# Kernel tuning notes

Measured on AMD Instinct MI355X. Metric: run time of the kernel, lower is better.

## Reference

```python
import jax, jax.numpy as jnp
import numpy as np

NUM_GENES = 8192
NUM_SETS = 256
BATCH = 32
ALPHA = 0.25


def setup_inputs() -> dict:
    key = jax.random.key(0)
    k1, k2, k3 = jax.random.split(key, 3)
    R = jax.random.uniform(k1, (BATCH, NUM_GENES), dtype=jnp.float32)
    # S is a per-sample permutation of gene indices (sort order)
    S = jnp.argsort(jax.random.uniform(k2, (BATCH, NUM_GENES)), axis=1).astype(jnp.int32)
    W = jax.random.normal(k3, (NUM_SETS, NUM_GENES), dtype=jnp.float32)  # set_membership
    return {"R": R, "S": S, "W": W}


def _set_indicators(W):
    ind = jax.nn.sigmoid(W)  # (M, G)
    avg = ind.mean(axis=1, keepdims=True)
    return jnp.where(ind < avg * 0.3, ind * 0.01, ind)


def reference(R, S, W):
    batch, num_genes = R.shape
    ind = _set_indicators(W)                                   # (M, G)
    # gather indicators per sample's sort order: (B, M, G)
    sorted_ind = jnp.transpose(ind[:, S], (1, 0, 2))
    R_sorted = jnp.take_along_axis(R, S, axis=1)               # (B, G)
    clamped = jnp.clip(R_sorted[:, None, :] * sorted_ind, 1e-8, 1e4)
    wpos = clamped ** ALPHA                                    # (B, M, G)
    sum_pos = jnp.sum(wpos, axis=2, keepdims=True)
    cdf_pos = jnp.where(sum_pos > 1e-8,
                        jnp.cumsum(wpos, axis=2) / (sum_pos + 1e-10),
                        jnp.zeros_like(wpos))
    neg = (sorted_ind < 0.1).astype(R.dtype)                   # (B, M, G)
    sum_neg = jnp.sum(neg, axis=2, keepdims=True)
    cdf_neg = jnp.where(sum_neg > 1e-8,
                        jnp.cumsum(neg, axis=2) / (sum_neg + 1e-10),
                        jnp.zeros_like(neg))
    diff = (cdf_pos - cdf_neg) / num_genes
    return jnp.sum(diff, axis=2)                               # (B, M)
```

## Files before the change

### kernel.cpp

```cpp
#include <hip/hip_runtime.h>
#include <math.h>

constexpr int NG  = 8192;
constexpr int NM  = 256;
constexpr int NB  = 32;
constexpr int KR  = 128;
constexpr int NKB = NG / KR;


using bf16x8 = __attribute__((ext_vector_type(8))) short;
using f32x4  = __attribute__((ext_vector_type(4))) float;

__device__ __forceinline__ float sigmoidf(float x) {
  return __builtin_amdgcn_rcpf(1.0f + __builtin_amdgcn_exp2f(x * -1.442695041f));
}
__device__ __forceinline__ float qrtf(float x) {
  return __builtin_amdgcn_sqrtf(__builtin_amdgcn_sqrtf(x));
}
__device__ __forceinline__ short bfr(float f) {
  unsigned x = __float_as_uint(f);
  return (short)((x + 0x7fffu + ((x >> 16) & 1u)) >> 16);
}

__global__ __launch_bounds__(256) void k_prep(const int* __restrict__ S,
                                              const float* __restrict__ W,
                                              float* __restrict__ cf,
                                              float* __restrict__ thr,
                                              float* __restrict__ sumN) {
  const int tid = threadIdx.x;

  if (blockIdx.x < NM) {
    __shared__ float red[4];
    const int m = blockIdx.x;
    const float4* w4 = reinterpret_cast<const float4*>(W + (size_t)m * NG);
    float4 sg[8];
    float s = 0.f;
    #pragma unroll
    for (int q = 0; q < 8; ++q) {
      float4 v = w4[q * 256 + tid];
      sg[q] = make_float4(sigmoidf(v.x), sigmoidf(v.y), sigmoidf(v.z), sigmoidf(v.w));
      s += sg[q].x + sg[q].y + sg[q].z + sg[q].w;
    }
    #pragma unroll
    for (int off = 32; off > 0; off >>= 1) s += __shfl_xor(s, off, 64);
    if ((tid & 63) == 0) red[tid >> 6] = s;
    __syncthreads();
    const float tm = (red[0] + red[1] + red[2] + red[3]) * (0.3f / (float)NG);
    __syncthreads();
    float sn = 0.f;
    #pragma unroll
    for (int q = 0; q < 8; ++q) {
      float vv[4] = {sg[q].x, sg[q].y, sg[q].z, sg[q].w};
      #pragma unroll
      for (int j = 0; j < 4; ++j) {
        float v = vv[j];
        v = (v < tm) ? v * 0.01f : v;
        sn += (v < 0.1f) ? 1.f : 0.f;
      }
    }
    #pragma unroll
    for (int off = 32; off > 0; off >>= 1) sn += __shfl_xor(sn, off, 64);
    if ((tid & 63) == 0) red[tid >> 6] = sn;
    __syncthreads();
    if (tid == 0) { thr[m] = tm; sumN[m] = red[0] + red[1] + red[2] + red[3]; }
  } else {
    __shared__ float row[NG];
    const int b = blockIdx.x - NM;
    const int4* s4 = reinterpret_cast<const int4*>(S + (size_t)b * NG);
    #pragma unroll
    for (int q = 0; q < 8; ++q) {
      const int i = q * 256 + tid;
      const int4 g4 = s4[i];
      const int k = i * 4;
      row[g4.x] = (float)(NG - k);
      row[g4.y] = (float)(NG - (k + 1));
      row[g4.z] = (float)(NG - (k + 2));
      row[g4.w] = (float)(NG - (k + 3));
    }
    __syncthreads();
    float4* dst = reinterpret_cast<float4*>(cf + (size_t)b * NG);
    const float4* src = reinterpret_cast<const float4*>(row);
    #pragma unroll
    for (int q = 0; q < 8; ++q)
      dst[q * 256 + tid] = src[q * 256 + tid];
  }
}

__global__ __launch_bounds__(256) void k_mm(const float* __restrict__ W,
                                            const float* __restrict__ thr,
                                            const float* __restrict__ R,
                                            const float* __restrict__ cf,
                                            float* __restrict__ part) {
  const int tid  = threadIdx.x;
  const int kb   = blockIdx.x;
  const int mt   = blockIdx.y;
  const int wv   = tid >> 6;
  const int mw   = wv >> 1, bw = wv & 1;
  const int lane = tid & 63;
  const int lr   = lane & 15, lk = lane >> 4;

  const int m = mt * 32 + mw * 16 + lr;
  const int b = bw * 16 + lr;
  const float tm = thr[m];

  f32x4 accA = {0.f, 0.f, 0.f, 0.f};
  f32x4 accB = {0.f, 0.f, 0.f, 0.f};
  f32x4 accC = {0.f, 0.f, 0.f, 0.f};

  #pragma unroll
  for (int c = 0; c < KR / 32; ++c) {
    const int g = kb * KR + c * 32 + lk * 8;

    const float4 w0 = *reinterpret_cast<const float4*>(W + (size_t)m * NG + g);
    const float4 w1 = *reinterpret_cast<const float4*>(W + (size_t)m * NG + g + 4);
    const float wa[8] = {w0.x, w0.y, w0.z, w0.w, w1.x, w1.y, w1.z, w1.w};
    bf16x8 fia, fnf;
    #pragma unroll
    for (int e = 0; e < 8; ++e) {
      float v = sigmoidf(wa[e]);
      v = (v < tm) ? v * 0.01f : v;
      fia[e] = bfr(qrtf(v));
      fnf[e] = (v < 0.1f) ? (short)0x3F80 : (short)0;
    }

    const float4 r0 = *reinterpret_cast<const float4*>(R  + (size_t)b * NG + g);
    const float4 r1 = *reinterpret_cast<const float4*>(R  + (size_t)b * NG + g + 4);
    const float4 c0 = *reinterpret_cast<const float4*>(cf + (size_t)b * NG + g);
    const float4 c1 = *reinterpret_cast<const float4*>(cf + (size_t)b * NG + g + 4);
    const float rr[8] = {r0.x, r0.y, r0.z, r0.w, r1.x, r1.y, r1.z, r1.w};
    const float cc[8] = {c0.x, c0.y, c0.z, c0.w, c1.x, c1.y, c1.z, c1.w};
    bf16x8 fra, frc, fcf;
    #pragma unroll
    for (int e = 0; e < 8; ++e) {
      const float ra = qrtf(rr[e]);
      fra[e] = bfr(ra);
      frc[e] = bfr(ra * cc[e]);
      fcf[e] = bfr(cc[e]);
    }

    accA = __builtin_amdgcn_mfma_f32_16x16x32_bf16(fia, fra, accA, 0, 0, 0);
    accB = __builtin_amdgcn_mfma_f32_16x16x32_bf16(fia, frc, accB, 0, 0, 0);
    accC = __builtin_amdgcn_mfma_f32_16x16x32_bf16(fnf, fcf, accC, 0, 0, 0);
  }

  const int md = mt * 32 + mw * 16 + 4 * lk;
  const int bd = bw * 16 + lr;
  #pragma unroll
  for (int i = 0; i < 4; ++i) {
    part[((size_t)(kb * 3 + 0) * NM + md + i) * NB + bd] = accA[i];
    part[((size_t)(kb * 3 + 1) * NM + md + i) * NB + bd] = accB[i];
    part[((size_t)(kb * 3 + 2) * NM + md + i) * NB + bd] = accC[i];
  }
}

__global__ __launch_bounds__(256) void k_final(const float* __restrict__ part,
                                               const float* __restrict__ sumN,
                                               float* __restrict__ out) {
  __shared__ float rA[256], rB[256], rC[256];
  const int tid = threadIdx.x;
  const int m   = blockIdx.x;
  const int b   = tid & 31;
  const int kg  = tid >> 5;

  float sA = 0.f, sB = 0.f, sC = 0.f;
  #pragma unroll
  for (int t = 0; t < NKB / 8; ++t) {
    const int kb = kg * (NKB / 8) + t;
    const float* p = part + ((size_t)(kb * 3) * NM + m) * NB + b;
    sA += p[0];
    sB += p[(size_t)NM * NB];
    sC += p[2 * (size_t)NM * NB];
  }
  rA[tid] = sA; rB[tid] = sB; rC[tid] = sC;
  __syncthreads();
  if (tid < 128) { rA[tid] += rA[tid + 128]; rB[tid] += rB[tid + 128]; rC[tid] += rC[tid + 128]; }
  __syncthreads();
  if (tid < 64)  { rA[tid] += rA[tid + 64];  rB[tid] += rB[tid + 64];  rC[tid] += rC[tid + 64]; }
  __syncthreads();
  if (tid < 32) {
    const float a  = rA[tid] + rA[tid + 32];
    const float bb = rB[tid] + rB[tid + 32];
    const float c  = rC[tid] + rC[tid + 32];
    const float sN = sumN[m];
    out[(size_t)tid * NM + m] = (bb / (a + 1e-10f) - c / (sN + 1e-10f)) * (1.0f / (float)NG);
  }
}

extern "C" void kernel_launch(void* const* d_in, const int* in_sizes, int n_in,
                              void* d_out, int out_size, void* d_ws, size_t ws_size,
                              hipStream_t stream) {
  const float* R = (const float*)d_in[0];
  const int*   S = (const int*)d_in[1];
  const float* W = (const float*)d_in[2];
  float* out = (float*)d_out;

  char* ws = (char*)d_ws;
  float* cf   = (float*)ws;
  float* part = cf + (size_t)NB * NG;
  float* thr  = part + (size_t)NKB * 3 * NM * NB;
  float* sumN = thr + NM;

  k_prep <<<dim3(NM + NB), dim3(256), 0, stream>>>(S, W, cf, thr, sumN);
  k_mm   <<<dim3(NKB, NM / 32), dim3(256), 0, stream>>>(W, thr, R, cf, part);
  k_final<<<dim3(NM), dim3(256), 0, stream>>>(part, sumN, out);
}
```

Measured before the change: 22.36 us.

## Precompute packed bf16 operands in prep kernel and double K-chunk size

The prep kernel now computes the transformed set indicators (fourth root in bf16, negative flag packed into the sign bit) and the per-sample bf16 operands (rank fourth root, its product with the rank-based CDF weight, the rank itself). It writes them to workspace, so the matmul kernel only loads bf16 vectors and does bit masking before the MFMAs. This removes the sigmoid, threshold and fourth-root work that k_mm repeated for every m-tile and batch half, and halves the bytes it reads. K-block size goes from 128 to 256, halving the partial-sum traffic but also the number of k_mm blocks. The cost is extra global writes and reads of the packed buffers.

```diff
diff --git a/kernel.cpp b/kernel.cpp
--- a/kernel.cpp
+++ b/kernel.cpp
@@ -4,11 +4,12 @@
 constexpr int NG  = 8192;
 constexpr int NM  = 256;
 constexpr int NB  = 32;
-constexpr int KR  = 128;
+constexpr int KR  = 256;
 constexpr int NKB = NG / KR;
 
 
 using bf16x8 = __attribute__((ext_vector_type(8))) short;
+using s16x4  = __attribute__((ext_vector_type(4))) short;
 using f32x4  = __attribute__((ext_vector_type(4))) float;
 
 __device__ __forceinline__ float sigmoidf(float x) {
@@ -24,8 +25,9 @@
 
 __global__ __launch_bounds__(256) void k_prep(const int* __restrict__ S,
                                               const float* __restrict__ W,
-                                              float* __restrict__ cf,
-                                              float* __restrict__ thr,
+                                              const float* __restrict__ R,
+                                              unsigned short* __restrict__ pA,
+                                              unsigned short* __restrict__ pB,
                                               float* __restrict__ sumN) {
   const int tid = threadIdx.x;
 
@@ -46,23 +48,27 @@
     if ((tid & 63) == 0) red[tid >> 6] = s;
     __syncthreads();
     const float tm = (red[0] + red[1] + red[2] + red[3]) * (0.3f / (float)NG);
-    __syncthreads();
     float sn = 0.f;
+    s16x4* dst = reinterpret_cast<s16x4*>(pA + (size_t)m * NG);
     #pragma unroll
     for (int q = 0; q < 8; ++q) {
       float vv[4] = {sg[q].x, sg[q].y, sg[q].z, sg[q].w};
+      s16x4 po;
       #pragma unroll
       for (int j = 0; j < 4; ++j) {
         float v = vv[j];
         v = (v < tm) ? v * 0.01f : v;
-        sn += (v < 0.1f) ? 1.f : 0.f;
+        const bool ng = v < 0.1f;
+        po[j] = (short)(bfr(qrtf(v)) | (ng ? (short)0x8000 : (short)0));
+        sn += ng ? 1.f : 0.f;
       }
+      dst[q * 256 + tid] = po;
     }
     #pragma unroll
     for (int off = 32; off > 0; off >>= 1) sn += __shfl_xor(sn, off, 64);
     if ((tid & 63) == 0) red[tid >> 6] = sn;
     __syncthreads();
-    if (tid == 0) { thr[m] = tm; sumN[m] = red[0] + red[1] + red[2] + red[3]; }
+    if (tid == 0) sumN[m] = red[0] + red[1] + red[2] + red[3];
   } else {
     __shared__ float row[NG];
     const int b = blockIdx.x - NM;
@@ -78,18 +84,33 @@
       row[g4.w] = (float)(NG - (k + 3));
     }
     __syncthreads();
-    float4* dst = reinterpret_cast<float4*>(cf + (size_t)b * NG);
-    const float4* src = reinterpret_cast<const float4*>(row);
-    #pragma unroll
-    for (int q = 0; q < 8; ++q)
-      dst[q * 256 + tid] = src[q * 256 + tid];
-  }
-}
-
-__global__ __launch_bounds__(256) void k_mm(const float* __restrict__ W,
-                                            const float* __restrict__ thr,
-                                            const float* __restrict__ R,
-                                            const float* __restrict__ cf,
+    const float4* r4 = reinterpret_cast<const float4*>(R + (size_t)b * NG);
+    const float4* c4 = reinterpret_cast<const float4*>(row);
+    s16x4* dra = reinterpret_cast<s16x4*>(pB + 0 * (size_t)NB * NG + (size_t)b * NG);
+    s16x4* drc = reinterpret_cast<s16x4*>(pB + 1 * (size_t)NB * NG + (size_t)b * NG);
+    s16x4* dcf = reinterpret_cast<s16x4*>(pB + 2 * (size_t)NB * NG + (size_t)b * NG);
+    #pragma unroll
+    for (int q = 0; q < 8; ++q) {
+      const float4 r = r4[q * 256 + tid];
+      const float4 c = c4[q * 256 + tid];
+      const float ra[4] = {qrtf(r.x), qrtf(r.y), qrtf(r.z), qrtf(r.w)};
+      const float cc[4] = {c.x, c.y, c.z, c.w};
+      s16x4 pra, prc, pcf;
+      #pragma unroll
+      for (int j = 0; j < 4; ++j) {
+        pra[j] = bfr(ra[j]);
+        prc[j] = bfr(ra[j] * cc[j]);
+        pcf[j] = bfr(cc[j]);
+      }
+      dra[q * 256 + tid] = pra;
+      drc[q * 256 + tid] = prc;
+      dcf[q * 256 + tid] = pcf;
+    }
+  }
+}
+
+__global__ __launch_bounds__(256) void k_mm(const unsigned short* __restrict__ pA,
+                                            const unsigned short* __restrict__ pB,
                                             float* __restrict__ part) {
   const int tid  = threadIdx.x;
   const int kb   = blockIdx.x;
@@ -101,7 +122,11 @@
 
   const int m = mt * 32 + mw * 16 + lr;
   const int b = bw * 16 + lr;
-  const float tm = thr[m];
+
+  const unsigned short* Arow = pA + (size_t)m * NG;
+  const unsigned short* Bra  = pB + 0 * (size_t)NB * NG + (size_t)b * NG;
+  const unsigned short* Brc  = pB + 1 * (size_t)NB * NG + (size_t)b * NG;
+  const unsigned short* Bcf  = pB + 2 * (size_t)NB * NG + (size_t)b * NG;
 
   f32x4 accA = {0.f, 0.f, 0.f, 0.f};
   f32x4 accB = {0.f, 0.f, 0.f, 0.f};
@@ -111,32 +136,20 @@
   for (int c = 0; c < KR / 32; ++c) {
     const int g = kb * KR + c * 32 + lk * 8;
 
-    const float4 w0 = *reinterpret_cast<const float4*>(W + (size_t)m * NG + g);
-    const float4 w1 = *reinterpret_cast<const float4*>(W + (size_t)m * NG + g + 4);
-    const float wa[8] = {w0.x, w0.y, w0.z, w0.w, w1.x, w1.y, w1.z, w1.w};
-    bf16x8 fia, fnf;
-    #pragma unroll
-    for (int e = 0; e < 8; ++e) {
-      float v = sigmoidf(wa[e]);
-      v = (v < tm) ? v * 0.01f : v;
-      fia[e] = bfr(qrtf(v));
-      fnf[e] = (v < 0.1f) ? (short)0x3F80 : (short)0;
-    }
-
-    const float4 r0 = *reinterpret_cast<const float4*>(R  + (size_t)b * NG + g);
-    const float4 r1 = *reinterpret_cast<const float4*>(R  + (size_t)b * NG + g + 4);
-    const float4 c0 = *reinterpret_cast<const float4*>(cf + (size_t)b * NG + g);
-    const float4 c1 = *reinterpret_cast<const float4*>(cf + (size_t)b * NG + g + 4);
-    const float rr[8] = {r0.x, r0.y, r0.z, r0.w, r1.x, r1.y, r1.z, r1.w};
-    const float cc[8] = {c0.x, c0.y, c0.z, c0.w, c1.x, c1.y, c1.z, c1.w};
-    bf16x8 fra, frc, fcf;
-    #pragma unroll
-    for (int e = 0; e < 8; ++e) {
-      const float ra = qrtf(rr[e]);
-      fra[e] = bfr(ra);
-      frc[e] = bfr(ra * cc[e]);
-      fcf[e] = bfr(cc[e]);
-    }
+    const int4 aw = *reinterpret_cast<const int4*>(Arow + g);
+    int4 iaw, nfw;
+    iaw.x = aw.x & 0x7FFF7FFF;  iaw.y = aw.y & 0x7FFF7FFF;
+    iaw.z = aw.z & 0x7FFF7FFF;  iaw.w = aw.w & 0x7FFF7FFF;
+    nfw.x = (int)(((unsigned)(aw.x & 0x80008000) >> 15) * 0x3F80u);
+    nfw.y = (int)(((unsigned)(aw.y & 0x80008000) >> 15) * 0x3F80u);
+    nfw.z = (int)(((unsigned)(aw.z & 0x80008000) >> 15) * 0x3F80u);
+    nfw.w = (int)(((unsigned)(aw.w & 0x80008000) >> 15) * 0x3F80u);
+    const bf16x8 fia = __builtin_bit_cast(bf16x8, iaw);
+    const bf16x8 fnf = __builtin_bit_cast(bf16x8, nfw);
+
+    const bf16x8 fra = *reinterpret_cast<const bf16x8*>(Bra + g);
+    const bf16x8 frc = *reinterpret_cast<const bf16x8*>(Brc + g);
+    const bf16x8 fcf = *reinterpret_cast<const bf16x8*>(Bcf + g);
 
     accA = __builtin_amdgcn_mfma_f32_16x16x32_bf16(fia, fra, accA, 0, 0, 0);
     accB = __builtin_amdgcn_mfma_f32_16x16x32_bf16(fia, frc, accB, 0, 0, 0);
@@ -195,12 +208,12 @@
   float* out = (float*)d_out;
 
   char* ws = (char*)d_ws;
-  float* cf   = (float*)ws;
-  float* part = cf + (size_t)NB * NG;
-  float* thr  = part + (size_t)NKB * 3 * NM * NB;
-  float* sumN = thr + NM;
-
-  k_prep <<<dim3(NM + NB), dim3(256), 0, stream>>>(S, W, cf, thr, sumN);
-  k_mm   <<<dim3(NKB, NM / 32), dim3(256), 0, stream>>>(W, thr, R, cf, part);
+  unsigned short* pA = (unsigned short*)ws;
+  unsigned short* pB = pA + (size_t)NM * NG;
+  float* part = (float*)(ws + (size_t)NM * NG * 2 + (size_t)3 * NB * NG * 2);
+  float* sumN = part + (size_t)NKB * 3 * NM * NB;
+
+  k_prep <<<dim3(NM + NB), dim3(256), 0, stream>>>(S, W, R, pA, pB, sumN);
+  k_mm   <<<dim3(NKB, NM / 32), dim3(256), 0, stream>>>(pA, pB, part);
   k_final<<<dim3(NM), dim3(256), 0, stream>>>(part, sumN, out);
 }
```

Result: faster. 20.41 us (-8.7%).
